# Optimization experiments

Hardware: AMD Instinct MI355X
Metric: run time of the kernel (lower is better)

Reference implementation:

```python
import jax, jax.numpy as jnp
import numpy as np

N = 50000      # nodes
E = 800000     # edges (before self-loops)
G = 64         # graphs
F_IN = 128
HID = 64
HEADS = 2
OUT = 10
NEG_SLOPE = 0.2


def setup_inputs() -> dict:
    key = jax.random.key(0)
    ks = jax.random.split(key, 12)
    x = jax.random.normal(ks[0], (N, F_IN), dtype=jnp.float32)
    edge_index = jax.random.randint(ks[1], (2, E), 0, N, dtype=jnp.int64)
    batch = jnp.sort(jax.random.randint(ks[2], (N,), 0, G, dtype=jnp.int64))
    s = 0.1
    params = {
        "W1": jax.random.normal(ks[3], (F_IN, HEADS * HID), dtype=jnp.float32) * s,
        "att_src1": jax.random.normal(ks[4], (HEADS, HID), dtype=jnp.float32) * s,
        "att_dst1": jax.random.normal(ks[5], (HEADS, HID), dtype=jnp.float32) * s,
        "b1": jnp.zeros((HEADS * HID,), dtype=jnp.float32),
        "W2": jax.random.normal(ks[6], (HEADS * HID, HEADS * HID), dtype=jnp.float32) * s,
        "att_src2": jax.random.normal(ks[7], (HEADS, HID), dtype=jnp.float32) * s,
        "att_dst2": jax.random.normal(ks[8], (HEADS, HID), dtype=jnp.float32) * s,
        "b2": jnp.zeros((HEADS * HID,), dtype=jnp.float32),
        "Wl": jax.random.normal(ks[9], (HEADS * HID, OUT), dtype=jnp.float32) * s,
        "bl": jnp.zeros((OUT,), dtype=jnp.float32),
    }
    return {"x": x, "edge_index": edge_index, "batch": batch, **params}


def gat_conv(x, W, att_src, att_dst, bias, src, dst):
    # x: [N, Fin]; W: [Fin, H*C]
    h = (x @ W).reshape(N, HEADS, HID)                      # [N, H, C]
    a_src = jnp.sum(h * att_src, axis=-1)                   # [N, H]
    a_dst = jnp.sum(h * att_dst, axis=-1)                   # [N, H]
    alpha = jax.nn.leaky_relu(a_src[src] + a_dst[dst], NEG_SLOPE)  # [Etot, H]
    # segment softmax over incoming edges of each dst node
    m = jax.ops.segment_max(alpha, dst, num_segments=N)     # [N, H]
    alpha = jnp.exp(alpha - m[dst])
    denom = jax.ops.segment_sum(alpha, dst, num_segments=N)
    alpha = alpha / (denom[dst] + 1e-16)
    out = jax.ops.segment_sum(alpha[:, :, None] * h[src], dst, num_segments=N)
    return out.reshape(N, HEADS * HID) + bias


def reference(x, edge_index, batch, W1, att_src1, att_dst1, b1,
              W2, att_src2, att_dst2, b2, Wl, bl):
    # PyG GATConv default: add self-loops
    loop = jnp.arange(N, dtype=edge_index.dtype)
    src = jnp.concatenate([edge_index[0], loop])
    dst = jnp.concatenate([edge_index[1], loop])

    h = jax.nn.relu(gat_conv(x, W1, att_src1, att_dst1, b1, src, dst))
    h = jax.nn.relu(gat_conv(h, W2, att_src2, att_dst2, b2, src, dst))

    # global_mean_pool over graphs
    sums = jax.ops.segment_sum(h, batch, num_segments=G)        # [G, H*C]
    cnts = jax.ops.segment_sum(jnp.ones((N,), h.dtype), batch, num_segments=G)
    pooled = sums / jnp.maximum(cnts, 1.0)[:, None]
    return pooled @ Wl + bl                                      # [G, OUT]
```

## Files before the change

### kernel.cpp

```cpp
#include <hip/hip_runtime.h>
#include <hip/hip_fp16.h>
#include <math.h>

#define N_NODES 50000
#define N_EDGES 800000
#define ETOT    850000
#define GRAPHS  64
#define FIN     128
#define HC      128
#define OUTF    10
#define NEG     0.2f

#define NBUCK   196
#define BCAP    8192
#define EPT     8
#define GEMMB   782
#define ABLK    416

using half8   = __attribute__((ext_vector_type(8))) _Float16;
using float4v = __attribute__((ext_vector_type(4))) float;

__global__ void setupk(const float* __restrict__ W1, const float* __restrict__ W2,
                       _Float16* __restrict__ WT1, _Float16* __restrict__ WT2,
                       int* __restrict__ tails, float* __restrict__ sums) {
    int i = blockIdx.x * 256 + threadIdx.x;
    if (i < 16384) {
        int n = i >> 7, k = i & 127;
        WT1[i] = (_Float16)W1[k * 128 + n];
        WT2[i] = (_Float16)W2[k * 128 + n];
    }
    if (i < NBUCK) tails[i] = 0;
    if (i < GRAPHS * HC) sums[i] = 0.f;
}

template<bool FP32IN>
__device__ __forceinline__ void gemm_body(int bid, int t, _Float16 (*wt)[128],
                                          const void* __restrict__ Xin,
                                          const _Float16* __restrict__ WT,
                                          const float* __restrict__ att_s,
                                          const float* __restrict__ att_d,
                                          _Float16* __restrict__ H16,
                                          float2* __restrict__ a_src,
                                          float2* __restrict__ a_dst) {
    for (int i = t; i < 128 * 16; i += 256) {
        int n = i >> 4, ch = i & 15;
        int k0 = ch * 8;
        half8 v = *(const half8*)&WT[n * 128 + k0];
        *(half8*)&wt[n][k0 ^ ((n & 7) << 3)] = v;
    }

    int w = t >> 6, lane = t & 63;
    int hi = lane >> 4, l16 = lane & 15;
    int rbase = bid * 64 + w * 16;
    int arow = min(rbase + l16, N_NODES - 1);

    half8 a[4];
    if (FP32IN) {
        const float* X = (const float*)Xin;
#pragma unroll
        for (int kb = 0; kb < 4; ++kb) {
            int k0 = kb * 32 + hi * 8;
            float4 x0 = *(const float4*)&X[(size_t)arow * 128 + k0];
            float4 x1 = *(const float4*)&X[(size_t)arow * 128 + k0 + 4];
            half8 v;
            v[0] = (_Float16)x0.x; v[1] = (_Float16)x0.y;
            v[2] = (_Float16)x0.z; v[3] = (_Float16)x0.w;
            v[4] = (_Float16)x1.x; v[5] = (_Float16)x1.y;
            v[6] = (_Float16)x1.z; v[7] = (_Float16)x1.w;
            a[kb] = v;
        }
    } else {
        const _Float16* X = (const _Float16*)Xin;
#pragma unroll
        for (int kb = 0; kb < 4; ++kb)
            a[kb] = *(const half8*)&X[(size_t)arow * 128 + kb * 32 + hi * 8];
    }

    __syncthreads();

    float4v acc[8];
#pragma unroll
    for (int ct = 0; ct < 8; ++ct) {
        float4v c = {0.f, 0.f, 0.f, 0.f};
        int n = ct * 16 + l16;
#pragma unroll
        for (int kb = 0; kb < 4; ++kb) {
            int k0 = (kb * 32 + hi * 8) ^ ((n & 7) << 3);
            half8 b = *(const half8*)&wt[n][k0];
            c = __builtin_amdgcn_mfma_f32_16x16x32_f16(a[kb], b, c, 0, 0, 0);
        }
        acc[ct] = c;
    }

    int grow0 = rbase + hi * 4;
#pragma unroll
    for (int ct = 0; ct < 8; ++ct) {
#pragma unroll
        for (int r = 0; r < 4; ++r) {
            int grow = grow0 + r;
            if (grow < N_NODES)
                H16[(size_t)grow * 128 + ct * 16 + l16] = (_Float16)acc[ct][r];
        }
    }

    float as_[8], ad_[8];
#pragma unroll
    for (int ct = 0; ct < 8; ++ct) {
        as_[ct] = att_s[ct * 16 + l16];
        ad_[ct] = att_d[ct * 16 + l16];
    }
#pragma unroll
    for (int r = 0; r < 4; ++r) {
        float s0 = 0.f, s1 = 0.f, d0 = 0.f, d1 = 0.f;
#pragma unroll
        for (int ct = 0; ct < 4; ++ct) { s0 += acc[ct][r] * as_[ct]; d0 += acc[ct][r] * ad_[ct]; }
#pragma unroll
        for (int ct = 4; ct < 8; ++ct) { s1 += acc[ct][r] * as_[ct]; d1 += acc[ct][r] * ad_[ct]; }
        for (int off = 1; off < 16; off <<= 1) {
            s0 += __shfl_xor(s0, off); s1 += __shfl_xor(s1, off);
            d0 += __shfl_xor(d0, off); d1 += __shfl_xor(d1, off);
        }
        int grow = grow0 + r;
        if (l16 == 0 && grow < N_NODES) {
            a_src[grow] = make_float2(s0, s1);
            a_dst[grow] = make_float2(d0, d1);
        }
    }
}

__device__ __forceinline__ void bucketA_body(int bid, int t,
                                             int* hist, int* lbase,
                                             const int* __restrict__ ei,
                                             int* __restrict__ tails,
                                             int* __restrict__ bdata) {
    int e0 = bid * (256 * EPT);
    for (int i = t; i < NBUCK; i += 256) hist[i] = 0;
    __syncthreads();

    int bb[EPT], pk[EPT], rk[EPT];
#pragma unroll
    for (int i = 0; i < EPT; ++i) {
        int e = e0 + i * 256 + t;
        bb[i] = -1;
        if (e < ETOT) {
            int s, d;
            if (e < N_EDGES) { s = ei[e]; d = ei[N_EDGES + e]; }
            else             { s = d = e - N_EDGES; }
            bb[i] = d >> 8;
            pk[i] = s | ((d & 255) << 16);
            rk[i] = atomicAdd(&hist[bb[i]], 1);
        }
    }
    __syncthreads();
    for (int i = t; i < NBUCK; i += 256)
        lbase[i] = atomicAdd(&tails[i], hist[i]);
    __syncthreads();
#pragma unroll
    for (int i = 0; i < EPT; ++i)
        if (bb[i] >= 0) bdata[bb[i] * BCAP + lbase[bb[i]] + rk[i]] = pk[i];
}

__global__ __launch_bounds__(256) void fusedA(const float* __restrict__ x,
                                              const _Float16* __restrict__ WT1,
                                              const float* __restrict__ att_s,
                                              const float* __restrict__ att_d,
                                              _Float16* __restrict__ H16,
                                              float2* __restrict__ a_src,
                                              float2* __restrict__ a_dst,
                                              const int* __restrict__ ei,
                                              int* __restrict__ tails,
                                              int* __restrict__ bdata) {
    __shared__ _Float16 wt[128][128];
    __shared__ int hist[NBUCK];
    __shared__ int lbase[NBUCK];
    int t = threadIdx.x;
    if (blockIdx.x < GEMMB) {
        gemm_body<true>(blockIdx.x, t, wt, x, WT1, att_s, att_d, H16, a_src, a_dst);
    } else {
        bucketA_body(blockIdx.x - GEMMB, t, hist, lbase, ei, tails, bdata);
    }
}

__global__ __launch_bounds__(256) void gemmMFMA(const _Float16* __restrict__ Xin,
                                                const _Float16* __restrict__ WT,
                                                const float* __restrict__ att_s,
                                                const float* __restrict__ att_d,
                                                _Float16* __restrict__ H16,
                                                float2* __restrict__ a_src,
                                                float2* __restrict__ a_dst) {
    __shared__ _Float16 wt[128][128];
    gemm_body<false>(blockIdx.x, threadIdx.x, wt, Xin, WT, att_s, att_d, H16, a_src, a_dst);
}

__global__ __launch_bounds__(256) void bucketB(const int* __restrict__ bdata,
                                               const int* __restrict__ tails,
                                               int* __restrict__ rowptr,
                                               int* __restrict__ csr) {
    __shared__ int hist[256];
    __shared__ int scanws[256];
    int b = blockIdx.x;
    int t = threadIdx.x;

    int cb = (t < NBUCK) ? tails[t] : 0;
    scanws[t] = cb;
    __syncthreads();
    for (int off = 1; off < 256; off <<= 1) {
        int add = (t >= off) ? scanws[t - off] : 0;
        __syncthreads();
        scanws[t] += add;
        __syncthreads();
    }
    int base = scanws[b] - tails[b];
    if (b == NBUCK - 1 && t == 0) rowptr[N_NODES] = scanws[NBUCK - 1];
    int cnt = tails[b];
    int nodes0 = b << 8;
    int nnodes = min(256, N_NODES - nodes0);
    const int* bd = &bdata[b * BCAP];
    __syncthreads();

    hist[t] = 0;
    __syncthreads();
    for (int j = t; j < cnt; j += 256) atomicAdd(&hist[bd[j] >> 16], 1);
    __syncthreads();
    scanws[t] = hist[t];
    __syncthreads();
    for (int off = 1; off < 256; off <<= 1) {
        int add = (t >= off) ? scanws[t - off] : 0;
        __syncthreads();
        scanws[t] += add;
        __syncthreads();
    }
    int excl = scanws[t] - hist[t];
    if (t < nnodes) rowptr[nodes0 + t] = base + excl;
    __syncthreads();
    hist[t] = excl;
    __syncthreads();
    for (int j = t; j < cnt; j += 256) {
        int pkv = bd[j];
        int pos = atomicAdd(&hist[pkv >> 16], 1);
        csr[base + pos] = pkv & 0xFFFF;
    }
}

__device__ __forceinline__ float leaky(float x) { return x > 0.f ? x : NEG * x; }

template<bool POOL>
__global__ __launch_bounds__(256) void aggk(const __half* __restrict__ H16,
                                            const float2* __restrict__ a_src,
                                            const float2* __restrict__ a_dst,
                                            const int* __restrict__ rowptr,
                                            const int* __restrict__ csr,
                                            const float* __restrict__ bias,
                                            _Float16* __restrict__ out16,
                                            const int* __restrict__ batch,
                                            float* __restrict__ sums) {
    __shared__ float pbuf[POOL ? 4 : 1][128];
    __shared__ int pg[4];
    int t = threadIdx.x;
    int wid = (blockIdx.x * 256 + t) >> 6;
    int w = t >> 6;
    int lane = t & 63;
    int rbeg = rowptr[wid], rend = rowptr[wid + 1];
    float2 ad = a_dst[wid];

    int grp = lane >> 4;
    int gl  = lane & 15;
    int head = gl >> 3;
    float adh = head ? ad.y : ad.x;
    int f = gl * 8;

    float acc[8] = {0.f, 0.f, 0.f, 0.f, 0.f, 0.f, 0.f, 0.f};
    float denom = 0.f;
#pragma unroll 2
    for (int j = rbeg + grp; j < rend; j += 4) {
        int s = csr[j];
        float2 as = a_src[s];
        float wgt = __expf(leaky((head ? as.y : as.x) + adh));
        uint4 raw = *(const uint4*)&H16[(size_t)s * 128 + f];
        float2 p;
        p = __half22float2(*(__half2*)&raw.x); acc[0] += wgt * p.x; acc[1] += wgt * p.y;
        p = __half22float2(*(__half2*)&raw.y); acc[2] += wgt * p.x; acc[3] += wgt * p.y;
        p = __half22float2(*(__half2*)&raw.z); acc[4] += wgt * p.x; acc[5] += wgt * p.y;
        p = __half22float2(*(__half2*)&raw.w); acc[6] += wgt * p.x; acc[7] += wgt * p.y;
        denom += wgt;
    }
#pragma unroll
    for (int off = 16; off <= 32; off <<= 1) {
#pragma unroll
        for (int i = 0; i < 8; ++i) acc[i] += __shfl_xor(acc[i], off);
        denom += __shfl_xor(denom, off);
    }

    float inv = 1.f / (denom + 1e-16f);
    if (POOL) {
        if (grp == 0) {
            if (gl == 0) pg[w] = batch[wid];
#pragma unroll
            for (int i = 0; i < 8; ++i)
                pbuf[w][f + i] = fmaxf(acc[i] * inv + bias[f + i], 0.f);
        }
        __syncthreads();
        if (t < 128) {
#pragma unroll
            for (int ws = 0; ws < 4; ++ws) {
                bool leader = true;
#pragma unroll
                for (int v = 0; v < ws; ++v) leader = leader && (pg[ws] != pg[v]);
                if (leader) {
                    float s = pbuf[ws][t];
#pragma unroll
                    for (int u = ws + 1; u < 4; ++u)
                        if (pg[u] == pg[ws]) s += pbuf[u][t];
                    atomicAdd(&sums[pg[ws] * 128 + t], s);
                }
            }
        }
    } else {
        if (grp == 0) {
            half8 h;
#pragma unroll
            for (int i = 0; i < 8; ++i)
                h[i] = (_Float16)fmaxf(acc[i] * inv + bias[f + i], 0.f);
            *(half8*)&out16[(size_t)wid * 128 + f] = h;
        }
    }
}

__global__ void finalk(const float* __restrict__ sums, const int* __restrict__ batch,
                       const float* __restrict__ Wl, const float* __restrict__ bl,
                       float* __restrict__ out) {
    int t = threadIdx.x;
    if (t >= GRAPHS * OUTF) return;
    int g = t / OUTF, o = t % OUTF;
    int lo = 0, hi = N_NODES;
    while (lo < hi) { int m = (lo + hi) >> 1; if (batch[m] < g) lo = m + 1; else hi = m; }
    int lb = lo;
    lo = 0; hi = N_NODES;
    while (lo < hi) { int m = (lo + hi) >> 1; if (batch[m] < g + 1) lo = m + 1; else hi = m; }
    float inv = 1.f / fmaxf((float)(lo - lb), 1.f);
    float acc = 0.f;
#pragma unroll 8
    for (int k = 0; k < 128; ++k) acc += sums[g * 128 + k] * Wl[k * OUTF + o];
    out[t] = acc * inv + bl[o];
}

extern "C" void kernel_launch(void* const* d_in, const int* in_sizes, int n_in,
                              void* d_out, int out_size, void* d_ws, size_t ws_size,
                              hipStream_t stream) {
    const float* x        = (const float*)d_in[0];
    const int*   ei       = (const int*)d_in[1];
    const int*   batch    = (const int*)d_in[2];
    const float* W1       = (const float*)d_in[3];
    const float* att_src1 = (const float*)d_in[4];
    const float* att_dst1 = (const float*)d_in[5];
    const float* b1       = (const float*)d_in[6];
    const float* W2       = (const float*)d_in[7];
    const float* att_src2 = (const float*)d_in[8];
    const float* att_dst2 = (const float*)d_in[9];
    const float* b2       = (const float*)d_in[10];
    const float* Wl       = (const float*)d_in[11];
    const float* bl       = (const float*)d_in[12];
    float* out = (float*)d_out;

    size_t off = 0;
    auto alloc = [&](size_t bytes) -> void* {
        void* p = (char*)d_ws + off;
        off = (off + bytes + 255) & ~(size_t)255;
        return p;
    };
    _Float16* H16     = (_Float16*)alloc((size_t)N_NODES * 128 * 2);
    _Float16* B16     = (_Float16*)alloc((size_t)N_NODES * 128 * 2);
    _Float16* WT1     = (_Float16*)alloc(16384 * 2);
    _Float16* WT2     = (_Float16*)alloc(16384 * 2);
    float2*   a_src   = (float2*)alloc((size_t)N_NODES * 8);
    float2*   a_dst   = (float2*)alloc((size_t)N_NODES * 8);
    int*      bdata   = (int*)alloc((size_t)NBUCK * BCAP * 4);
    int*      tails   = (int*)alloc(NBUCK * 4);
    int*      rowptr  = (int*)alloc((size_t)(N_NODES + 1) * 4);
    int*      csr     = (int*)alloc((size_t)ETOT * 4);
    float*    sums    = (float*)alloc((size_t)GRAPHS * HC * 4);

    const int waveBlocks = (N_NODES * 64 + 255) / 256;

    setupk<<<64, 256, 0, stream>>>(W1, W2, WT1, WT2, tails, sums);
    fusedA<<<GEMMB + ABLK, 256, 0, stream>>>(x, WT1, att_src1, att_dst1,
                                             H16, a_src, a_dst, ei, tails, bdata);
    bucketB<<<NBUCK, 256, 0, stream>>>(bdata, tails, rowptr, csr);
    aggk<false><<<waveBlocks, 256, 0, stream>>>((const __half*)H16, a_src, a_dst,
                                                rowptr, csr, b1, B16, batch, sums);
    gemmMFMA<<<GEMMB, 256, 0, stream>>>(B16, WT2, att_src2, att_dst2,
                                        H16, a_src, a_dst);
    aggk<true><<<waveBlocks, 256, 0, stream>>>((const __half*)H16, a_src, a_dst,
                                               rowptr, csr, b2, nullptr, batch, sums);
    finalk<<<1, 640, 0, stream>>>(sums, batch, Wl, bl, out);
}
```

Baseline: 160.5 us.

## Slice feature matrices into four 32-column planes and split aggregation per slice

Stores H16 and B16 as four column-slices of 32 halves per node, laid out slice-major, so each aggregation block handles one slice for four destination nodes. Each slice's gather footprint is about a quarter of the full feature matrix, which is meant to improve cache hit rate on random neighbour gathers. It also uses 16 edge groups per wave instead of 4, and loads CSR with nontemporal hints. The cost is that each slice recomputes the attention weights and re-reads CSR four times, and the pooling atomics are split into four times as many blocks.

```diff
diff --git a/kernel.cpp b/kernel.cpp
--- a/kernel.cpp
+++ b/kernel.cpp
@@ -19,6 +19,7 @@
 
 using half8   = __attribute__((ext_vector_type(8))) _Float16;
 using float4v = __attribute__((ext_vector_type(4))) float;
+
 
 __global__ void setupk(const float* __restrict__ W1, const float* __restrict__ W2,
                        _Float16* __restrict__ WT1, _Float16* __restrict__ WT2,
@@ -73,7 +74,7 @@
         const _Float16* X = (const _Float16*)Xin;
 #pragma unroll
         for (int kb = 0; kb < 4; ++kb)
-            a[kb] = *(const half8*)&X[(size_t)arow * 128 + kb * 32 + hi * 8];
+            a[kb] = *(const half8*)&X[((size_t)kb * N_NODES + arow) * 32 + hi * 8];
     }
 
     __syncthreads();
@@ -95,11 +96,13 @@
     int grow0 = rbase + hi * 4;
 #pragma unroll
     for (int ct = 0; ct < 8; ++ct) {
+        int sl = ct >> 1;
+        int cc = (ct & 1) * 16 + l16;
 #pragma unroll
         for (int r = 0; r < 4; ++r) {
             int grow = grow0 + r;
             if (grow < N_NODES)
-                H16[(size_t)grow * 128 + ct * 16 + l16] = (_Float16)acc[ct][r];
+                H16[((size_t)sl * N_NODES + grow) * 32 + cc] = (_Float16)acc[ct][r];
         }
     }
 
@@ -245,7 +248,7 @@
 __device__ __forceinline__ float leaky(float x) { return x > 0.f ? x : NEG * x; }
 
 template<bool POOL>
-__global__ __launch_bounds__(256) void aggk(const __half* __restrict__ H16,
+__global__ __launch_bounds__(256) void aggk(const _Float16* __restrict__ H16,
                                             const float2* __restrict__ a_src,
                                             const float2* __restrict__ a_dst,
                                             const int* __restrict__ rowptr,
@@ -254,29 +257,32 @@
                                             _Float16* __restrict__ out16,
                                             const int* __restrict__ batch,
                                             float* __restrict__ sums) {
-    __shared__ float pbuf[POOL ? 4 : 1][128];
+    __shared__ float pbuf[POOL ? 4 : 1][32];
     __shared__ int pg[4];
     int t = threadIdx.x;
-    int wid = (blockIdx.x * 256 + t) >> 6;
+    int bid = blockIdx.x;
+    int slice = bid & 3;
     int w = t >> 6;
+    int wid = (bid >> 2) * 4 + w;
     int lane = t & 63;
     int rbeg = rowptr[wid], rend = rowptr[wid + 1];
     float2 ad = a_dst[wid];
 
-    int grp = lane >> 4;
-    int gl  = lane & 15;
-    int head = gl >> 3;
+    int grp = lane >> 2;
+    int gl  = lane & 3;
+    int head = slice >> 1;
     float adh = head ? ad.y : ad.x;
     int f = gl * 8;
 
+    const _Float16* Hs = &H16[(size_t)slice * N_NODES * 32];
+
     float acc[8] = {0.f, 0.f, 0.f, 0.f, 0.f, 0.f, 0.f, 0.f};
     float denom = 0.f;
-#pragma unroll 2
-    for (int j = rbeg + grp; j < rend; j += 4) {
-        int s = csr[j];
+    for (int j = rbeg + grp; j < rend; j += 16) {
+        int s = __builtin_nontemporal_load(&csr[j]);
         float2 as = a_src[s];
         float wgt = __expf(leaky((head ? as.y : as.x) + adh));
-        uint4 raw = *(const uint4*)&H16[(size_t)s * 128 + f];
+        uint4 raw = *(const uint4*)&Hs[(size_t)s * 32 + f];
         float2 p;
         p = __half22float2(*(__half2*)&raw.x); acc[0] += wgt * p.x; acc[1] += wgt * p.y;
         p = __half22float2(*(__half2*)&raw.y); acc[2] += wgt * p.x; acc[3] += wgt * p.y;
@@ -285,7 +291,7 @@
         denom += wgt;
     }
 #pragma unroll
-    for (int off = 16; off <= 32; off <<= 1) {
+    for (int off = 4; off <= 32; off <<= 1) {
 #pragma unroll
         for (int i = 0; i < 8; ++i) acc[i] += __shfl_xor(acc[i], off);
         denom += __shfl_xor(denom, off);
@@ -297,10 +303,10 @@
             if (gl == 0) pg[w] = batch[wid];
 #pragma unroll
             for (int i = 0; i < 8; ++i)
-                pbuf[w][f + i] = fmaxf(acc[i] * inv + bias[f + i], 0.f);
+                pbuf[w][f + i] = fmaxf(acc[i] * inv + bias[slice * 32 + f + i], 0.f);
         }
         __syncthreads();
-        if (t < 128) {
+        if (t < 32) {
 #pragma unroll
             for (int ws = 0; ws < 4; ++ws) {
                 bool leader = true;
@@ -311,7 +317,7 @@
 #pragma unroll
                     for (int u = ws + 1; u < 4; ++u)
                         if (pg[u] == pg[ws]) s += pbuf[u][t];
-                    atomicAdd(&sums[pg[ws] * 128 + t], s);
+                    atomicAdd(&sums[pg[ws] * 128 + slice * 32 + t], s);
                 }
             }
         }
@@ -320,8 +326,8 @@
             half8 h;
 #pragma unroll
             for (int i = 0; i < 8; ++i)
-                h[i] = (_Float16)fmaxf(acc[i] * inv + bias[f + i], 0.f);
-            *(half8*)&out16[(size_t)wid * 128 + f] = h;
+                h[i] = (_Float16)fmaxf(acc[i] * inv + bias[slice * 32 + f + i], 0.f);
+            *(half8*)&out16[((size_t)slice * N_NODES + wid) * 32 + f] = h;
         }
     }
 }
@@ -380,17 +386,17 @@
     int*      csr     = (int*)alloc((size_t)ETOT * 4);
     float*    sums    = (float*)alloc((size_t)GRAPHS * HC * 4);
 
-    const int waveBlocks = (N_NODES * 64 + 255) / 256;
+    const int aggBlocks = N_NODES;
 
     setupk<<<64, 256, 0, stream>>>(W1, W2, WT1, WT2, tails, sums);
     fusedA<<<GEMMB + ABLK, 256, 0, stream>>>(x, WT1, att_src1, att_dst1,
                                              H16, a_src, a_dst, ei, tails, bdata);
     bucketB<<<NBUCK, 256, 0, stream>>>(bdata, tails, rowptr, csr);
-    aggk<false><<<waveBlocks, 256, 0, stream>>>((const __half*)H16, a_src, a_dst,
-                                                rowptr, csr, b1, B16, batch, sums);
+    aggk<false><<<aggBlocks, 256, 0, stream>>>(H16, a_src, a_dst,
+                                               rowptr, csr, b1, B16, batch, sums);
     gemmMFMA<<<GEMMB, 256, 0, stream>>>(B16, WT2, att_src2, att_dst2,
                                         H16, a_src, a_dst);
-    aggk<true><<<waveBlocks, 256, 0, stream>>>((const __half*)H16, a_src, a_dst,
-                                               rowptr, csr, b2, nullptr, batch, sums);
+    aggk<true><<<aggBlocks, 256, 0, stream>>>(H16, a_src, a_dst,
+                                              rowptr, csr, b2, nullptr, batch, sums);
     finalk<<<1, 640, 0, stream>>>(sums, batch, Wl, bl, out);
 }
```

Measured after the change: 281.4 us. 1.75x slower.
